# Performance work log

Hardware: AMD Instinct MI355X
Metric: run time of the kernel (lower is better)

Reference implementation:

```python
import jax, jax.numpy as jnp
import numpy as np

B, N, E = 32, 128, 16384
D, H, O, A = 72, 72, 72, 4   # n_input, n_hidden, n_output, n_node_attr
C_WEIGHT = 1.0
EPS = 1e-5  # BatchNorm1d default eps


def setup_inputs() -> dict:
    key = jax.random.key(0)
    ks = jax.random.split(key, 16)
    rn = lambda k, shp, s=0.05: jax.random.normal(k, shp, jnp.float32) * s
    return {
        "h": jax.random.normal(ks[0], (B, N, D), jnp.float32),
        "x": jax.random.normal(ks[1], (B, N, 4), jnp.float32),
        "edgei": jax.random.randint(ks[2], (B, E), 0, N),
        "edgej": jax.random.randint(ks[3], (B, E), 0, N),
        "node_attr": jax.random.normal(ks[4], (B, N, A), jnp.float32),
        # phi_e: Linear(2D+2 -> H, no bias), BN, ReLU, Linear(H->H), ReLU
        "We1": rn(ks[5], (2 * D + 2, H)),
        "g1": jnp.ones((H,), jnp.float32), "b1": jnp.zeros((H,), jnp.float32),
        "We2": rn(ks[6], (H, H)), "be2": jnp.zeros((H,), jnp.float32),
        # phi_m: Linear(H->1), Sigmoid
        "Wm": rn(ks[7], (H, 1)), "bm": jnp.zeros((1,), jnp.float32),
        # phi_x: Linear(H->H), ReLU, Linear(H->1, no bias, tiny init)
        "Wx1": rn(ks[8], (H, H)), "bx1": jnp.zeros((H,), jnp.float32),
        "Wx2": rn(ks[9], (H, 1), 0.001),
        # phi_h: Linear(H+D+A -> H), BN, ReLU, Linear(H->O)
        "Wh1": rn(ks[10], (H + D + A, H)), "bh1": jnp.zeros((H,), jnp.float32),
        "gh": jnp.ones((H,), jnp.float32), "bh": jnp.zeros((H,), jnp.float32),
        "Wh2": rn(ks[11], (H, O)), "bh2": jnp.zeros((O,), jnp.float32),
    }


def _psi(p):
    return jnp.sign(p) * jnp.log1p(jnp.abs(p))


def _normsq4(p):  # Minkowski norm: p0^2 - p1^2 - p2^2 - p3^2
    psq = p * p
    return 2.0 * psq[..., 0] - psq.sum(axis=-1)


def _dotsq4(p, q):  # Minkowski inner product
    pq = p * q
    return 2.0 * pq[..., 0] - pq.sum(axis=-1)


def _batchnorm(z, g, b):  # training-mode BatchNorm1d over flattened batch dim
    mu = z.mean(axis=0)
    var = z.var(axis=0)
    return (z - mu) * jax.lax.rsqrt(var + EPS) * g + b


_seg_sum = jax.vmap(lambda d, s: jax.ops.segment_sum(d, s, num_segments=N))


def reference(h, x, edgei, edgej, node_attr,
              We1, g1, b1, We2, be2, Wm, bm,
              Wx1, bx1, Wx2, Wh1, bh1, gh, bh, Wh2, bh2):
    # gather edge endpoint features (equiv. to torch.gather along dim 1)
    xi = jnp.take_along_axis(x, edgei[:, :, None], axis=1)    # [B,E,4]
    xj = jnp.take_along_axis(x, edgej[:, :, None], axis=1)
    hi = jnp.take_along_axis(h, edgei[:, :, None], axis=1)    # [B,E,D]
    hj = jnp.take_along_axis(h, edgej[:, :, None], axis=1)
    x_diff = xi - xj
    norms = _psi(_normsq4(x_diff))[..., None]                 # [B,E,1]
    dots = _psi(_dotsq4(xi, xj))[..., None]                   # [B,E,1]

    # m_model: phi_e then sigmoid gate phi_m
    feat = jnp.concatenate([hi, hj, norms, dots], axis=-1)    # [B,E,2D+2]
    z = feat.reshape(-1, 2 * D + 2) @ We1
    z = jax.nn.relu(_batchnorm(z, g1, b1))
    z = jax.nn.relu(z @ We2 + be2)
    m = z.reshape(B, E, H)
    m = m * jax.nn.sigmoid(m @ Wm + bm)                       # gated messages

    # x_model: equivariant coordinate update (segment mean over edges)
    gate = jax.nn.relu(m @ Wx1 + bx1) @ Wx2                   # [B,E,1]
    trans = jnp.clip(x_diff * gate, -100.0, 100.0)
    agg = _seg_sum(trans, edgei)                              # [B,N,4]
    cnt = _seg_sum(jnp.ones_like(trans), edgei)
    x_out = x + (agg / jnp.maximum(cnt, 1.0)) * C_WEIGHT

    # h_model: segment sum of messages, node MLP, residual
    magg = _seg_sum(m, edgei)                                 # [B,N,H]
    hin = jnp.concatenate([h, magg, node_attr], axis=-1).reshape(-1, H + D + A)
    z2 = hin @ Wh1 + bh1
    z2 = jax.nn.relu(_batchnorm(z2, gh, bh))
    z2 = z2 @ Wh2 + bh2
    h_out = h + z2.reshape(B, N, O)

    return (h_out, x_out, m)
```

## Files before the change

### kernel.cpp

```cpp
#include <hip/hip_runtime.h>

#define BB 32
#define NN 128
#define EE 16384
#define ROWS_E (BB*EE)
#define ROWS_N (BB*NN)
#define EPS_BN 1e-5f

#define XOUT_OFF (ROWS_N*72)
#define M_OFF    (XOUT_OFF + ROWS_N*4)

#define ST1_OFF 0
#define ST2_OFF 512
#define AGG_OFF 1024
#define CNT_OFF (AGG_OFF + ROWS_N*4)
#define MAGG_OFF (CNT_OFF + ROWS_N)
#define Z2_OFF (MAGG_OFF + ROWS_N*72)
#define ZERO_FLOATS Z2_OFF
#define WB_OFF (Z2_OFF + ROWS_N*72)

#define WE1T_OFF 0
#define WE2T_OFF 13440
#define WX1T_OFF 21760
#define WH1T_OFF 30080
#define WH2T_OFF 43520
#define WB_TOTAL 51840

typedef __attribute__((ext_vector_type(8))) short short8;
typedef __attribute__((ext_vector_type(4))) float f32x4;

__device__ __forceinline__ float psi_f(float p) {
    return copysignf(log1pf(fabsf(p)), p);
}
__device__ __forceinline__ unsigned short f2bf(float f) {
    union { float f; unsigned u; } v; v.f = f;
    unsigned r = v.u + 0x7fffu + ((v.u >> 16) & 1u);
    return (unsigned short)(r >> 16);
}
__device__ __forceinline__ unsigned pk(float a, float b) {
    return (unsigned)f2bf(a) | ((unsigned)f2bf(b) << 16);
}

__global__ void k_prep(const float* __restrict__ We1, const float* __restrict__ We2,
                       const float* __restrict__ Wx1, const float* __restrict__ Wh1,
                       const float* __restrict__ Wh2, unsigned short* __restrict__ wb)
{
    int idx = blockIdx.x * 256 + threadIdx.x;
    if (idx >= WB_TOTAL) return;
    const float* src; int off, n, k, K;
    if (idx < WE2T_OFF)      { off = idx;            n = off/168; k = off%168; src = We1; K = 146; }
    else if (idx < WH1T_OFF && idx >= WX1T_OFF) { off = idx - WX1T_OFF; n = off/104; k = off%104; src = Wx1; K = 72; }
    else if (idx < WX1T_OFF) { off = idx - WE2T_OFF; n = off/104; k = off%104; src = We2; K = 72; }
    else if (idx < WH2T_OFF) { off = idx - WH1T_OFF; n = off/168; k = off%168; src = Wh1; K = 148; }
    else                     { off = idx - WH2T_OFF; n = off/104; k = off%104; src = Wh2; K = 72; }
    float v = (n < 72 && k < K) ? src[k * 72 + n] : 0.f;
    wb[idx] = f2bf(v);
}

__global__ __launch_bounds__(256) void k_edge_gemm1(
    const float* __restrict__ h, const float* __restrict__ x,
    const int* __restrict__ ei, const int* __restrict__ ej,
    const unsigned short* __restrict__ We1t, float* __restrict__ z1)
{
    __shared__ unsigned short At[128 * 168];
    __shared__ unsigned short Wt[80 * 168];
    int tid = threadIdx.x;
    {
        const uint4* s = (const uint4*)We1t; uint4* d = (uint4*)Wt;
        for (int q = tid; q < 1680; q += 256) d[q] = s[q];
    }
    int rl = tid >> 1, half = tid & 1;
    int row = blockIdx.x * 128 + rl;
    int b = row >> 14;
    int i = ei[row], j = ej[row];
    int node = half ? j : i;
    const float4* hp = (const float4*)(h + (size_t)(b * 128 + node) * 72);
    uint2* arow = (uint2*)(&At[rl * 168 + half * 72]);
    #pragma unroll
    for (int q = 0; q < 18; q++) {
        float4 v = hp[q];
        arow[q] = make_uint2(pk(v.x, v.y), pk(v.z, v.w));
    }
    unsigned* tailp = (unsigned*)(&At[rl * 168 + 146]);
    if (half == 0) {
        float4 xi = *(const float4*)(x + (size_t)(b * 128 + i) * 4);
        float4 xj = *(const float4*)(x + (size_t)(b * 128 + j) * 4);
        float d0 = xi.x - xj.x, d1 = xi.y - xj.y, d2 = xi.z - xj.z, d3 = xi.w - xj.w;
        float nrm = d0*d0 - d1*d1 - d2*d2 - d3*d3;
        float dot = xi.x*xj.x - xi.y*xj.y - xi.z*xj.z - xi.w*xj.w;
        *(unsigned*)(&At[rl * 168 + 144]) = pk(psi_f(nrm), psi_f(dot));
        #pragma unroll
        for (int q = 0; q < 6; q++) tailp[q] = 0u;
    } else {
        #pragma unroll
        for (int q = 6; q < 11; q++) tailp[q] = 0u;
    }
    __syncthreads();

    int wv = tid >> 6, lane = tid & 63, c = lane & 15, quad = lane >> 4;
    f32x4 acc[2][5] = {};
    for (int kc = 0; kc < 5; kc++) {
        int k0 = kc * 32 + quad * 8;
        short8 a0 = *(const short8*)(&At[(wv * 32 + c) * 168 + k0]);
        short8 a1 = *(const short8*)(&At[(wv * 32 + 16 + c) * 168 + k0]);
        #pragma unroll
        for (int ct = 0; ct < 5; ct++) {
            short8 bf = *(const short8*)(&Wt[(ct * 16 + c) * 168 + k0]);
            acc[0][ct] = __builtin_amdgcn_mfma_f32_16x16x32_bf16(a0, bf, acc[0][ct], 0, 0, 0);
            acc[1][ct] = __builtin_amdgcn_mfma_f32_16x16x32_bf16(a1, bf, acc[1][ct], 0, 0, 0);
        }
    }
    size_t rbase = (size_t)blockIdx.x * 128 + wv * 32 + quad * 4;
    #pragma unroll
    for (int rt = 0; rt < 2; rt++)
        #pragma unroll
        for (int ct = 0; ct < 5; ct++) {
            int col = ct * 16 + c;
            if (col < 72) {
                float* op = z1 + (rbase + rt * 16) * 72 + col;
                #pragma unroll
                for (int r = 0; r < 4; r++) op[(size_t)r * 72] = acc[rt][ct][r];
            }
        }
}

__global__ void k_stats(const float* __restrict__ z, int rows, float* __restrict__ st)
{
    __shared__ float ssum[4][72];
    __shared__ float ssq[4][72];
    int c = threadIdx.x, ty = threadIdx.y;
    float s = 0.f, q = 0.f;
    for (int r = blockIdx.x * 4 + ty; r < rows; r += gridDim.x * 4) {
        float v = z[(size_t)r * 72 + c];
        s += v; q += v * v;
    }
    ssum[ty][c] = s; ssq[ty][c] = q;
    __syncthreads();
    if (ty == 0) {
        s = ssum[0][c] + ssum[1][c] + ssum[2][c] + ssum[3][c];
        q = ssq[0][c] + ssq[1][c] + ssq[2][c] + ssq[3][c];
        atomicAdd(&st[c], s);
        atomicAdd(&st[72 + c], q);
    }
}

__global__ void k_finalize(float* __restrict__ st, float inv_rows)
{
    int c = threadIdx.x;
    if (c < 72) {
        float mean = st[c] * inv_rows;
        float var  = st[72 + c] * inv_rows - mean * mean;
        st[144 + c] = mean;
        st[216 + c] = rsqrtf(var + EPS_BN);
    }
}

__global__ __launch_bounds__(256) void k_edge_main(
    const float* __restrict__ x, const int* __restrict__ ei, const int* __restrict__ ej,
    const float* __restrict__ st1, const float* __restrict__ g1, const float* __restrict__ b1,
    const float* __restrict__ be2, const float* __restrict__ Wm, const float* __restrict__ bm,
    const float* __restrict__ bx1, const float* __restrict__ Wx2,
    const unsigned short* __restrict__ We2t, const unsigned short* __restrict__ Wx1t,
    float* __restrict__ m, float* __restrict__ agg, float* __restrict__ cnt)
{
    __shared__ unsigned short Zt[128 * 104];
    __shared__ unsigned short W2[80 * 104];
    __shared__ unsigned short W3[80 * 104];
    __shared__ float g2buf[128];
    int tid = threadIdx.x;
    {
        const uint4* s2 = (const uint4*)We2t; uint4* d2 = (uint4*)W2;
        const uint4* s3 = (const uint4*)Wx1t; uint4* d3 = (uint4*)W3;
        for (int q = tid; q < 1040; q += 256) { d2[q] = s2[q]; d3[q] = s3[q]; }
    }
    int rl = tid >> 1, half = tid & 1;
    size_t row = (size_t)blockIdx.x * 128 + rl;
    const float* mean = st1 + 144;
    const float* inv  = st1 + 216;
    const float4* zp = (const float4*)(m + row * 72) + half * 9;
    uint2* arow = (uint2*)(&Zt[rl * 104 + half * 36]);
    #pragma unroll
    for (int q = 0; q < 9; q++) {
        int k = half * 36 + q * 4;
        float4 v = zp[q];
        float a0 = fmaxf((v.x - mean[k  ]) * inv[k  ] * g1[k  ] + b1[k  ], 0.f);
        float a1 = fmaxf((v.y - mean[k+1]) * inv[k+1] * g1[k+1] + b1[k+1], 0.f);
        float a2 = fmaxf((v.z - mean[k+2]) * inv[k+2] * g1[k+2] + b1[k+2], 0.f);
        float a3 = fmaxf((v.w - mean[k+3]) * inv[k+3] * g1[k+3] + b1[k+3], 0.f);
        arow[q] = make_uint2(pk(a0, a1), pk(a2, a3));
    }
    uint2* prow = (uint2*)(&Zt[rl * 104]);
    #pragma unroll
    for (int q = 0; q < 4; q++) prow[18 + half * 4 + q] = make_uint2(0u, 0u);
    __syncthreads();

    int wv = tid >> 6, lane = tid & 63, c = lane & 15, quad = lane >> 4;
    f32x4 acc2[2][5] = {};
    for (int kc = 0; kc < 3; kc++) {
        int k0 = kc * 32 + quad * 8;
        short8 a0 = *(const short8*)(&Zt[(wv * 32 + c) * 104 + k0]);
        short8 a1 = *(const short8*)(&Zt[(wv * 32 + 16 + c) * 104 + k0]);
        #pragma unroll
        for (int ct = 0; ct < 5; ct++) {
            short8 bf = *(const short8*)(&W2[(ct * 16 + c) * 104 + k0]);
            acc2[0][ct] = __builtin_amdgcn_mfma_f32_16x16x32_bf16(a0, bf, acc2[0][ct], 0, 0, 0);
            acc2[1][ct] = __builtin_amdgcn_mfma_f32_16x16x32_bf16(a1, bf, acc2[1][ct], 0, 0, 0);
        }
    }
    float part[2][4] = {};
    float bm0 = bm[0];
    #pragma unroll
    for (int ct = 0; ct < 5; ct++) {
        int col = ct * 16 + c;
        float bias = (col < 72) ? be2[col] : 0.f;
        float wm   = (col < 72) ? Wm[col]  : 0.f;
        #pragma unroll
        for (int rt = 0; rt < 2; rt++)
            #pragma unroll
            for (int r = 0; r < 4; r++) {
                float t = fmaxf(acc2[rt][ct][r] + bias, 0.f);
                acc2[rt][ct][r] = t;
                part[rt][r] += t * wm;
            }
    }
    float sg[2][4];
    #pragma unroll
    for (int rt = 0; rt < 2; rt++)
        #pragma unroll
        for (int r = 0; r < 4; r++) {
            float s = part[rt][r];
            s += __shfl_xor(s, 1); s += __shfl_xor(s, 2);
            s += __shfl_xor(s, 4); s += __shfl_xor(s, 8);
            sg[rt][r] = 1.f / (1.f + expf(-(s + bm0)));
        }
    size_t rbase = (size_t)blockIdx.x * 128 + wv * 32 + quad * 4;
    #pragma unroll
    for (int rt = 0; rt < 2; rt++)
        #pragma unroll
        for (int ct = 0; ct < 5; ct++) {
            int col = ct * 16 + c;
            #pragma unroll
            for (int r = 0; r < 4; r++) {
                float mv = acc2[rt][ct][r] * sg[rt][r];
                int lrow = wv * 32 + rt * 16 + quad * 4 + r;
                Zt[lrow * 104 + col] = f2bf(mv);
                if (col < 72) m[(rbase + rt * 16 + r) * 72 + col] = mv;
            }
        }
    f32x4 acc3[2][5] = {};
    for (int kc = 0; kc < 3; kc++) {
        int k0 = kc * 32 + quad * 8;
        short8 a0 = *(const short8*)(&Zt[(wv * 32 + c) * 104 + k0]);
        short8 a1 = *(const short8*)(&Zt[(wv * 32 + 16 + c) * 104 + k0]);
        #pragma unroll
        for (int ct = 0; ct < 5; ct++) {
            short8 bf = *(const short8*)(&W3[(ct * 16 + c) * 104 + k0]);
            acc3[0][ct] = __builtin_amdgcn_mfma_f32_16x16x32_bf16(a0, bf, acc3[0][ct], 0, 0, 0);
            acc3[1][ct] = __builtin_amdgcn_mfma_f32_16x16x32_bf16(a1, bf, acc3[1][ct], 0, 0, 0);
        }
    }
    float part3[2][4] = {};
    #pragma unroll
    for (int ct = 0; ct < 5; ct++) {
        int col = ct * 16 + c;
        float bias = (col < 72) ? bx1[col] : 0.f;
        float wx   = (col < 72) ? Wx2[col] : 0.f;
        #pragma unroll
        for (int rt = 0; rt < 2; rt++)
            #pragma unroll
            for (int r = 0; r < 4; r++)
                part3[rt][r] += fmaxf(acc3[rt][ct][r] + bias, 0.f) * wx;
    }
    #pragma unroll
    for (int rt = 0; rt < 2; rt++)
        #pragma unroll
        for (int r = 0; r < 4; r++) {
            float s = part3[rt][r];
            s += __shfl_xor(s, 1); s += __shfl_xor(s, 2);
            s += __shfl_xor(s, 4); s += __shfl_xor(s, 8);
            if (c == 0) g2buf[wv * 32 + rt * 16 + quad * 4 + r] = s;
        }
    __syncthreads();
    if (tid < 128) {
        size_t erow = (size_t)blockIdx.x * 128 + tid;
        int b = (int)(erow >> 14);
        int i2 = ei[erow], j2 = ej[erow];
        float g2 = g2buf[tid];
        float4 xi = *(const float4*)(x + (size_t)(b * 128 + i2) * 4);
        float4 xj = *(const float4*)(x + (size_t)(b * 128 + j2) * 4);
        float t0 = fminf(fmaxf((xi.x - xj.x) * g2, -100.f), 100.f);
        float t1 = fminf(fmaxf((xi.y - xj.y) * g2, -100.f), 100.f);
        float t2 = fminf(fmaxf((xi.z - xj.z) * g2, -100.f), 100.f);
        float t3 = fminf(fmaxf((xi.w - xj.w) * g2, -100.f), 100.f);
        float* ap = agg + (size_t)(b * 128 + i2) * 4;
        atomicAdd(ap + 0, t0); atomicAdd(ap + 1, t1);
        atomicAdd(ap + 2, t2); atomicAdd(ap + 3, t3);
        atomicAdd(cnt + (size_t)(b * 128 + i2), 1.f);
    }
}

__global__ __launch_bounds__(256) void k_magg(
    const float* __restrict__ m, const int* __restrict__ ei, float* __restrict__ magg)
{
    __shared__ float accum[128 * 72];
    int tid = threadIdx.x;
    for (int q = tid; q < 9216; q += 256) accum[q] = 0.f;
    __syncthreads();
    int b = blockIdx.x >> 3, chunk = blockIdx.x & 7;
    int wv = tid >> 6, lane = tid & 63;
    int ebase = b * 16384 + chunk * 2048;
    for (int e = wv; e < 2048; e += 4) {
        int erow = ebase + e;
        int node = ei[erow];
        const float* mr = m + (size_t)erow * 72;
        atomicAdd(&accum[node * 72 + lane], mr[lane]);
        if (lane < 8) atomicAdd(&accum[node * 72 + 64 + lane], mr[64 + lane]);
    }
    __syncthreads();
    float* mg = magg + (size_t)b * 9216;
    for (int q = tid; q < 9216; q += 256) atomicAdd(&mg[q], accum[q]);
}

__global__ __launch_bounds__(256) void k_node_gemm1(
    const float* __restrict__ h, const float* __restrict__ node_attr,
    const float* __restrict__ magg, const unsigned short* __restrict__ Wh1t,
    const float* __restrict__ bh1, float* __restrict__ z2)
{
    __shared__ unsigned short At[128 * 168];
    __shared__ unsigned short Wt[80 * 168];
    int tid = threadIdx.x;
    {
        const uint4* s = (const uint4*)Wh1t; uint4* d = (uint4*)Wt;
        for (int q = tid; q < 1680; q += 256) d[q] = s[q];
    }
    int rl = tid >> 1, half = tid & 1;
    size_t row = (size_t)blockIdx.x * 128 + rl;
    const float4* sp = (const float4*)((half ? magg : h) + row * 72);
    uint2* arow = (uint2*)(&At[rl * 168 + half * 72]);
    #pragma unroll
    for (int q = 0; q < 18; q++) {
        float4 v = sp[q];
        arow[q] = make_uint2(pk(v.x, v.y), pk(v.z, v.w));
    }
    if (half) {
        float4 na = *(const float4*)(node_attr + row * 4);
        *(unsigned*)(&At[rl * 168 + 144]) = pk(na.x, na.y);
        *(unsigned*)(&At[rl * 168 + 146]) = pk(na.z, na.w);
        unsigned* tailp = (unsigned*)(&At[rl * 168 + 148]);
        #pragma unroll
        for (int q = 0; q < 10; q++) tailp[q] = 0u;
    }
    __syncthreads();

    int wv = tid >> 6, lane = tid & 63, c = lane & 15, quad = lane >> 4;
    f32x4 acc[2][5] = {};
    for (int kc = 0; kc < 5; kc++) {
        int k0 = kc * 32 + quad * 8;
        short8 a0 = *(const short8*)(&At[(wv * 32 + c) * 168 + k0]);
        short8 a1 = *(const short8*)(&At[(wv * 32 + 16 + c) * 168 + k0]);
        #pragma unroll
        for (int ct = 0; ct < 5; ct++) {
            short8 bf = *(const short8*)(&Wt[(ct * 16 + c) * 168 + k0]);
            acc[0][ct] = __builtin_amdgcn_mfma_f32_16x16x32_bf16(a0, bf, acc[0][ct], 0, 0, 0);
            acc[1][ct] = __builtin_amdgcn_mfma_f32_16x16x32_bf16(a1, bf, acc[1][ct], 0, 0, 0);
        }
    }
    size_t rbase = (size_t)blockIdx.x * 128 + wv * 32 + quad * 4;
    #pragma unroll
    for (int rt = 0; rt < 2; rt++)
        #pragma unroll
        for (int ct = 0; ct < 5; ct++) {
            int col = ct * 16 + c;
            if (col < 72) {
                float bias = bh1[col];
                float* op = z2 + (rbase + rt * 16) * 72 + col;
                #pragma unroll
                for (int r = 0; r < 4; r++) op[(size_t)r * 72] = acc[rt][ct][r] + bias;
            }
        }
}

__global__ __launch_bounds__(256) void k_node_final(
    const float* __restrict__ h, const float* __restrict__ x,
    const float* __restrict__ z2, const float* __restrict__ st2,
    const float* __restrict__ gh, const float* __restrict__ bh,
    const unsigned short* __restrict__ Wh2t, const float* __restrict__ bh2,
    const float* __restrict__ agg, const float* __restrict__ cnt,
    float* __restrict__ hout, float* __restrict__ xout)
{
    __shared__ unsigned short Zt[128 * 104];
    __shared__ unsigned short Wt[80 * 104];
    int tid = threadIdx.x;
    {
        const uint4* s = (const uint4*)Wh2t; uint4* d = (uint4*)Wt;
        for (int q = tid; q < 1040; q += 256) d[q] = s[q];
    }
    int rl = tid >> 1, half = tid & 1;
    size_t row = (size_t)blockIdx.x * 128 + rl;
    const float* mean = st2 + 144;
    const float* inv  = st2 + 216;
    const float4* zp = (const float4*)(z2 + row * 72) + half * 9;
    uint2* arow = (uint2*)(&Zt[rl * 104 + half * 36]);
    #pragma unroll
    for (int q = 0; q < 9; q++) {
        int k = half * 36 + q * 4;
        float4 v = zp[q];
        float a0 = fmaxf((v.x - mean[k  ]) * inv[k  ] * gh[k  ] + bh[k  ], 0.f);
        float a1 = fmaxf((v.y - mean[k+1]) * inv[k+1] * gh[k+1] + bh[k+1], 0.f);
        float a2 = fmaxf((v.z - mean[k+2]) * inv[k+2] * gh[k+2] + bh[k+2], 0.f);
        float a3 = fmaxf((v.w - mean[k+3]) * inv[k+3] * gh[k+3] + bh[k+3], 0.f);
        arow[q] = make_uint2(pk(a0, a1), pk(a2, a3));
    }
    uint2* prow = (uint2*)(&Zt[rl * 104]);
    #pragma unroll
    for (int q = 0; q < 4; q++) prow[18 + half * 4 + q] = make_uint2(0u, 0u);
    __syncthreads();

    int wv = tid >> 6, lane = tid & 63, c = lane & 15, quad = lane >> 4;
    f32x4 acc[2][5] = {};
    for (int kc = 0; kc < 3; kc++) {
        int k0 = kc * 32 + quad * 8;
        short8 a0 = *(const short8*)(&Zt[(wv * 32 + c) * 104 + k0]);
        short8 a1 = *(const short8*)(&Zt[(wv * 32 + 16 + c) * 104 + k0]);
        #pragma unroll
        for (int ct = 0; ct < 5; ct++) {
            short8 bf = *(const short8*)(&Wt[(ct * 16 + c) * 104 + k0]);
            acc[0][ct] = __builtin_amdgcn_mfma_f32_16x16x32_bf16(a0, bf, acc[0][ct], 0, 0, 0);
            acc[1][ct] = __builtin_amdgcn_mfma_f32_16x16x32_bf16(a1, bf, acc[1][ct], 0, 0, 0);
        }
    }
    size_t rbase = (size_t)blockIdx.x * 128 + wv * 32 + quad * 4;
    #pragma unroll
    for (int rt = 0; rt < 2; rt++)
        #pragma unroll
        for (int ct = 0; ct < 5; ct++) {
            int col = ct * 16 + c;
            if (col < 72) {
                float bias = bh2[col];
                #pragma unroll
                for (int r = 0; r < 4; r++) {
                    size_t gr = (rbase + rt * 16 + r);
                    hout[gr * 72 + col] = h[gr * 72 + col] + acc[rt][ct][r] + bias;
                }
            }
        }
    if (tid < 128) {
        size_t nrow = (size_t)blockIdx.x * 128 + tid;
        float cn = fmaxf(cnt[nrow], 1.f);
        float4 ag = *(const float4*)(agg + nrow * 4);
        float4 xv = *(const float4*)(x + nrow * 4);
        ((float4*)xout)[nrow] = make_float4(xv.x + ag.x / cn, xv.y + ag.y / cn,
                                            xv.z + ag.z / cn, xv.w + ag.w / cn);
    }
}

extern "C" void kernel_launch(void* const* d_in, const int* in_sizes, int n_in,
                              void* d_out, int out_size, void* d_ws, size_t ws_size,
                              hipStream_t stream)
{
    const float* h   = (const float*)d_in[0];
    const float* x   = (const float*)d_in[1];
    const int*   ei  = (const int*)d_in[2];
    const int*   ej  = (const int*)d_in[3];
    const float* na  = (const float*)d_in[4];
    const float* We1 = (const float*)d_in[5];
    const float* g1  = (const float*)d_in[6];
    const float* b1  = (const float*)d_in[7];
    const float* We2 = (const float*)d_in[8];
    const float* be2 = (const float*)d_in[9];
    const float* Wm  = (const float*)d_in[10];
    const float* bm  = (const float*)d_in[11];
    const float* Wx1 = (const float*)d_in[12];
    const float* bx1 = (const float*)d_in[13];
    const float* Wx2 = (const float*)d_in[14];
    const float* Wh1 = (const float*)d_in[15];
    const float* bh1 = (const float*)d_in[16];
    const float* gh  = (const float*)d_in[17];
    const float* bhp = (const float*)d_in[18];
    const float* Wh2 = (const float*)d_in[19];
    const float* bh2 = (const float*)d_in[20];

    float* out  = (float*)d_out;
    float* hout = out;
    float* xout = out + XOUT_OFF;
    float* m    = out + M_OFF;
    float* ws   = (float*)d_ws;
    float* st1  = ws + ST1_OFF;
    float* st2  = ws + ST2_OFF;
    float* agg  = ws + AGG_OFF;
    float* cnt  = ws + CNT_OFF;
    float* magg = ws + MAGG_OFF;
    float* z2   = ws + Z2_OFF;
    unsigned short* wb = (unsigned short*)(ws + WB_OFF);

    hipMemsetAsync(d_ws, 0, (size_t)ZERO_FLOATS * sizeof(float), stream);
    k_prep<<<(WB_TOTAL + 255) / 256, 256, 0, stream>>>(We1, We2, Wx1, Wh1, Wh2, wb);
    k_edge_gemm1<<<ROWS_E / 128, 256, 0, stream>>>(h, x, ei, ej, wb + WE1T_OFF, m);
    k_stats<<<dim3(1024), dim3(72, 4), 0, stream>>>(m, ROWS_E, st1);
    k_finalize<<<1, 128, 0, stream>>>(st1, 1.0f / (float)ROWS_E);
    k_edge_main<<<ROWS_E / 128, 256, 0, stream>>>(x, ei, ej, st1, g1, b1, be2, Wm, bm,
                                                  bx1, Wx2, wb + WE2T_OFF, wb + WX1T_OFF,
                                                  m, agg, cnt);
    k_magg<<<256, 256, 0, stream>>>(m, ei, magg);
    k_node_gemm1<<<ROWS_N / 128, 256, 0, stream>>>(h, na, magg, wb + WH1T_OFF, bh1, z2);
    k_stats<<<dim3(16), dim3(72, 4), 0, stream>>>(z2, ROWS_N, st2);
    k_finalize<<<1, 128, 0, stream>>>(st2, 1.0f / (float)ROWS_N);
    k_node_final<<<ROWS_N / 128, 256, 0, stream>>>(h, x, z2, st2, gh, bhp,
                                                   wb + WH2T_OFF, bh2, agg, cnt, hout, xout);
}
```

Before: 783.0 us.

## Store BN pre-activations in bf16 and feed MFMA operands from registers

The edge GEMM kernels now gather edge features straight into MFMA B-operand registers in transposed (weight-as-A) form, and read weights from global memory. This removes the big LDS staging tiles and their syncs. When the workspace is large enough, the first-layer pre-activation z1 goes to a separate bf16 buffer instead of fp32 in the output. That halves the traffic for the stats pass and for the edge_main read, with a new bf16 stats kernel. BatchNorm scale and shift are folded into per-channel S/T in finalize. The trade-off is that stats are computed on rounded bf16 values, and weights are fetched from global or cache instead of LDS.

```diff
diff --git a/kernel.cpp b/kernel.cpp
--- a/kernel.cpp
+++ b/kernel.cpp
@@ -1,4 +1,5 @@
 #include <hip/hip_runtime.h>
+#include <hip/hip_bf16.h>
 
 #define BB 32
 #define NN 128
@@ -18,6 +19,8 @@
 #define Z2_OFF (MAGG_OFF + ROWS_N*72)
 #define ZERO_FLOATS Z2_OFF
 #define WB_OFF (Z2_OFF + ROWS_N*72)
+#define Z1BF_OFF 637248
+#define Z1BF_NEED ((size_t)(Z1BF_OFF + ROWS_E*72/2) * 4)
 
 #define WE1T_OFF 0
 #define WE2T_OFF 13440
@@ -38,7 +41,12 @@
     return (unsigned short)(r >> 16);
 }
 __device__ __forceinline__ unsigned pk(float a, float b) {
-    return (unsigned)f2bf(a) | ((unsigned)f2bf(b) << 16);
+    union { __hip_bfloat162 h; unsigned u; } cv;
+    cv.h = __float22bfloat162_rn(make_float2(a, b));
+    return cv.u;
+}
+__device__ __forceinline__ float bfu2f(unsigned u) {
+    union { unsigned u; float f; } v; v.u = u << 16; return v.f;
 }
 
 __global__ void k_prep(const float* __restrict__ We1, const float* __restrict__ We2,
@@ -47,81 +55,100 @@
 {
     int idx = blockIdx.x * 256 + threadIdx.x;
     if (idx >= WB_TOTAL) return;
-    const float* src; int off, n, k, K;
-    if (idx < WE2T_OFF)      { off = idx;            n = off/168; k = off%168; src = We1; K = 146; }
-    else if (idx < WH1T_OFF && idx >= WX1T_OFF) { off = idx - WX1T_OFF; n = off/104; k = off%104; src = Wx1; K = 72; }
-    else if (idx < WX1T_OFF) { off = idx - WE2T_OFF; n = off/104; k = off%104; src = We2; K = 72; }
-    else if (idx < WH2T_OFF) { off = idx - WH1T_OFF; n = off/168; k = off%168; src = Wh1; K = 148; }
-    else                     { off = idx - WH2T_OFF; n = off/104; k = off%104; src = Wh2; K = 72; }
+    const float* src; int off = idx, n, k, K;
+    if (off < WE2T_OFF)      {                  n = off/168; k = off%168; src = We1; K = 146; }
+    else if (off < WX1T_OFF) { off -= WE2T_OFF; n = off/104; k = off%104; src = We2; K = 72; }
+    else if (off < WH1T_OFF) { off -= WX1T_OFF; n = off/104; k = off%104; src = Wx1; K = 72; }
+    else if (off < WH2T_OFF) { off -= WH1T_OFF; n = off/168; k = off%168; src = Wh1; K = 148; }
+    else                     { off -= WH2T_OFF; n = off/104; k = off%104; src = Wh2; K = 72; }
     float v = (n < 72 && k < K) ? src[k * 72 + n] : 0.f;
     wb[idx] = f2bf(v);
 }
 
+template<bool BF>
 __global__ __launch_bounds__(256) void k_edge_gemm1(
     const float* __restrict__ h, const float* __restrict__ x,
     const int* __restrict__ ei, const int* __restrict__ ej,
-    const unsigned short* __restrict__ We1t, float* __restrict__ z1)
-{
-    __shared__ unsigned short At[128 * 168];
-    __shared__ unsigned short Wt[80 * 168];
+    const unsigned short* __restrict__ We1t, void* __restrict__ z1v)
+{
     int tid = threadIdx.x;
-    {
-        const uint4* s = (const uint4*)We1t; uint4* d = (uint4*)Wt;
-        for (int q = tid; q < 1680; q += 256) d[q] = s[q];
-    }
-    int rl = tid >> 1, half = tid & 1;
-    int row = blockIdx.x * 128 + rl;
-    int b = row >> 14;
-    int i = ei[row], j = ej[row];
-    int node = half ? j : i;
-    const float4* hp = (const float4*)(h + (size_t)(b * 128 + node) * 72);
-    uint2* arow = (uint2*)(&At[rl * 168 + half * 72]);
-    #pragma unroll
-    for (int q = 0; q < 18; q++) {
-        float4 v = hp[q];
-        arow[q] = make_uint2(pk(v.x, v.y), pk(v.z, v.w));
-    }
-    unsigned* tailp = (unsigned*)(&At[rl * 168 + 146]);
-    if (half == 0) {
-        float4 xi = *(const float4*)(x + (size_t)(b * 128 + i) * 4);
-        float4 xj = *(const float4*)(x + (size_t)(b * 128 + j) * 4);
-        float d0 = xi.x - xj.x, d1 = xi.y - xj.y, d2 = xi.z - xj.z, d3 = xi.w - xj.w;
-        float nrm = d0*d0 - d1*d1 - d2*d2 - d3*d3;
-        float dot = xi.x*xj.x - xi.y*xj.y - xi.z*xj.z - xi.w*xj.w;
-        *(unsigned*)(&At[rl * 168 + 144]) = pk(psi_f(nrm), psi_f(dot));
-        #pragma unroll
-        for (int q = 0; q < 6; q++) tailp[q] = 0u;
-    } else {
-        #pragma unroll
-        for (int q = 6; q < 11; q++) tailp[q] = 0u;
-    }
-    __syncthreads();
-
     int wv = tid >> 6, lane = tid & 63, c = lane & 15, quad = lane >> 4;
+    int blk = blockIdx.x;
+    int b = blk >> 7;
+    size_t ebase = (size_t)blk * 128 + wv * 32;
+    const float* hb = h + (size_t)b * 128 * 72;
+
+    int iN[2], jN[2];
+    #pragma unroll
+    for (int nt = 0; nt < 2; nt++) {
+        size_t e = ebase + nt * 16 + c;
+        iN[nt] = ei[e]; jN[nt] = ej[e];
+    }
+
     f32x4 acc[2][5] = {};
+    #pragma unroll
     for (int kc = 0; kc < 5; kc++) {
         int k0 = kc * 32 + quad * 8;
-        short8 a0 = *(const short8*)(&At[(wv * 32 + c) * 168 + k0]);
-        short8 a1 = *(const short8*)(&At[(wv * 32 + 16 + c) * 168 + k0]);
-        #pragma unroll
-        for (int ct = 0; ct < 5; ct++) {
-            short8 bf = *(const short8*)(&Wt[(ct * 16 + c) * 168 + k0]);
-            acc[0][ct] = __builtin_amdgcn_mfma_f32_16x16x32_bf16(a0, bf, acc[0][ct], 0, 0, 0);
-            acc[1][ct] = __builtin_amdgcn_mfma_f32_16x16x32_bf16(a1, bf, acc[1][ct], 0, 0, 0);
-        }
-    }
-    size_t rbase = (size_t)blockIdx.x * 128 + wv * 32 + quad * 4;
-    #pragma unroll
-    for (int rt = 0; rt < 2; rt++)
-        #pragma unroll
-        for (int ct = 0; ct < 5; ct++) {
-            int col = ct * 16 + c;
-            if (col < 72) {
-                float* op = z1 + (rbase + rt * 16) * 72 + col;
-                #pragma unroll
-                for (int r = 0; r < 4; r++) op[(size_t)r * 72] = acc[rt][ct][r];
+        int ch = kc * 4 + quad;
+        short8 bfr[2];
+        #pragma unroll
+        for (int nt = 0; nt < 2; nt++) {
+            if (ch < 18) {
+                const float* p = hb + (ch < 9 ? iN[nt] * 72 + ch * 8
+                                              : jN[nt] * 72 + (ch - 9) * 8);
+                float4 p0 = *(const float4*)p;
+                float4 p1 = *(const float4*)(p + 4);
+                short8 t;
+                unsigned u0 = pk(p0.x, p0.y), u1 = pk(p0.z, p0.w);
+                unsigned u2 = pk(p1.x, p1.y), u3 = pk(p1.z, p1.w);
+                t[0] = (short)(u0 & 0xffff); t[1] = (short)(u0 >> 16);
+                t[2] = (short)(u1 & 0xffff); t[3] = (short)(u1 >> 16);
+                t[4] = (short)(u2 & 0xffff); t[5] = (short)(u2 >> 16);
+                t[6] = (short)(u3 & 0xffff); t[7] = (short)(u3 >> 16);
+                bfr[nt] = t;
+            } else if (ch == 18) {
+                float4 xi = *(const float4*)(x + (size_t)(b * 128 + iN[nt]) * 4);
+                float4 xj = *(const float4*)(x + (size_t)(b * 128 + jN[nt]) * 4);
+                float d0 = xi.x-xj.x, d1 = xi.y-xj.y, d2 = xi.z-xj.z, d3 = xi.w-xj.w;
+                float nrm = d0*d0 - d1*d1 - d2*d2 - d3*d3;
+                float dot = xi.x*xj.x - xi.y*xj.y - xi.z*xj.z - xi.w*xj.w;
+                unsigned u = pk(psi_f(nrm), psi_f(dot));
+                short8 t = {0,0,0,0,0,0,0,0};
+                t[0] = (short)(u & 0xffff); t[1] = (short)(u >> 16);
+                bfr[nt] = t;
+            } else {
+                short8 t = {0,0,0,0,0,0,0,0};
+                bfr[nt] = t;
             }
         }
+        #pragma unroll
+        for (int mt = 0; mt < 5; mt++) {
+            short8 w = *(const short8*)(We1t + (mt * 16 + c) * 168 + k0);
+            acc[0][mt] = __builtin_amdgcn_mfma_f32_16x16x32_bf16(w, bfr[0], acc[0][mt], 0, 0, 0);
+            acc[1][mt] = __builtin_amdgcn_mfma_f32_16x16x32_bf16(w, bfr[1], acc[1][mt], 0, 0, 0);
+        }
+    }
+    #pragma unroll
+    for (int nt = 0; nt < 2; nt++) {
+        size_t e = ebase + nt * 16 + c;
+        #pragma unroll
+        for (int mt = 0; mt < 5; mt++) {
+            int col0 = mt * 16 + quad * 4;
+            if (col0 < 72) {
+                if (BF) {
+                    unsigned short* z1bf = (unsigned short*)z1v;
+                    *(uint2*)(z1bf + e * 72 + col0) =
+                        make_uint2(pk(acc[nt][mt][0], acc[nt][mt][1]),
+                                   pk(acc[nt][mt][2], acc[nt][mt][3]));
+                } else {
+                    float* z1f = (float*)z1v;
+                    *(float4*)(z1f + e * 72 + col0) =
+                        make_float4(acc[nt][mt][0], acc[nt][mt][1],
+                                    acc[nt][mt][2], acc[nt][mt][3]);
+                }
+            }
+        }
+    }
 }
 
 __global__ void k_stats(const float* __restrict__ z, int rows, float* __restrict__ st)
@@ -144,148 +171,210 @@
     }
 }
 
-__global__ void k_finalize(float* __restrict__ st, float inv_rows)
+__global__ void k_stats_bf(const unsigned* __restrict__ z1u, float* __restrict__ st)
+{
+    __shared__ float ssum[7][72];
+    __shared__ float ssq[7][72];
+    int p = threadIdx.x;
+    int ty = threadIdx.y;
+    float s0 = 0.f, s1 = 0.f, q0 = 0.f, q1 = 0.f;
+    for (int r = blockIdx.x * 7 + ty; r < ROWS_E; r += gridDim.x * 7) {
+        unsigned v = z1u[(size_t)r * 36 + p];
+        float a = bfu2f(v & 0xffffu);
+        float bb = bfu2f(v >> 16);
+        s0 += a; q0 += a * a; s1 += bb; q1 += bb * bb;
+    }
+    ssum[ty][2*p] = s0; ssum[ty][2*p+1] = s1;
+    ssq[ty][2*p] = q0;  ssq[ty][2*p+1] = q1;
+    __syncthreads();
+    if (ty == 0) {
+        #pragma unroll
+        for (int hh = 0; hh < 2; hh++) {
+            int col = 2*p + hh;
+            float s = 0.f, q = 0.f;
+            #pragma unroll
+            for (int t = 0; t < 7; t++) { s += ssum[t][col]; q += ssq[t][col]; }
+            atomicAdd(&st[col], s);
+            atomicAdd(&st[72 + col], q);
+        }
+    }
+}
+
+__global__ void k_finalize(float* __restrict__ st, float inv_rows,
+                           const float* __restrict__ g, const float* __restrict__ b)
 {
     int c = threadIdx.x;
     if (c < 72) {
         float mean = st[c] * inv_rows;
         float var  = st[72 + c] * inv_rows - mean * mean;
+        float rst  = rsqrtf(var + EPS_BN);
         st[144 + c] = mean;
-        st[216 + c] = rsqrtf(var + EPS_BN);
-    }
-}
-
+        st[216 + c] = rst;
+        float S = rst * g[c];
+        st[288 + c] = S;
+        st[360 + c] = b[c] - mean * S;
+    }
+}
+
+template<bool BF>
 __global__ __launch_bounds__(256) void k_edge_main(
-    const float* __restrict__ x, const int* __restrict__ ei, const int* __restrict__ ej,
-    const float* __restrict__ st1, const float* __restrict__ g1, const float* __restrict__ b1,
-    const float* __restrict__ be2, const float* __restrict__ Wm, const float* __restrict__ bm,
+    const void* __restrict__ z1v, const float* __restrict__ x,
+    const int* __restrict__ ei, const int* __restrict__ ej,
+    const float* __restrict__ st1, const float* __restrict__ be2,
+    const float* __restrict__ Wm, const float* __restrict__ bm,
     const float* __restrict__ bx1, const float* __restrict__ Wx2,
     const unsigned short* __restrict__ We2t, const unsigned short* __restrict__ Wx1t,
     float* __restrict__ m, float* __restrict__ agg, float* __restrict__ cnt)
 {
-    __shared__ unsigned short Zt[128 * 104];
-    __shared__ unsigned short W2[80 * 104];
-    __shared__ unsigned short W3[80 * 104];
-    __shared__ float g2buf[128];
+    __shared__ unsigned short mtile[128 * 72];
     int tid = threadIdx.x;
-    {
-        const uint4* s2 = (const uint4*)We2t; uint4* d2 = (uint4*)W2;
-        const uint4* s3 = (const uint4*)Wx1t; uint4* d3 = (uint4*)W3;
-        for (int q = tid; q < 1040; q += 256) { d2[q] = s2[q]; d3[q] = s3[q]; }
-    }
-    int rl = tid >> 1, half = tid & 1;
-    size_t row = (size_t)blockIdx.x * 128 + rl;
-    const float* mean = st1 + 144;
-    const float* inv  = st1 + 216;
-    const float4* zp = (const float4*)(m + row * 72) + half * 9;
-    uint2* arow = (uint2*)(&Zt[rl * 104 + half * 36]);
-    #pragma unroll
-    for (int q = 0; q < 9; q++) {
-        int k = half * 36 + q * 4;
-        float4 v = zp[q];
-        float a0 = fmaxf((v.x - mean[k  ]) * inv[k  ] * g1[k  ] + b1[k  ], 0.f);
-        float a1 = fmaxf((v.y - mean[k+1]) * inv[k+1] * g1[k+1] + b1[k+1], 0.f);
-        float a2 = fmaxf((v.z - mean[k+2]) * inv[k+2] * g1[k+2] + b1[k+2], 0.f);
-        float a3 = fmaxf((v.w - mean[k+3]) * inv[k+3] * g1[k+3] + b1[k+3], 0.f);
-        arow[q] = make_uint2(pk(a0, a1), pk(a2, a3));
-    }
-    uint2* prow = (uint2*)(&Zt[rl * 104]);
-    #pragma unroll
-    for (int q = 0; q < 4; q++) prow[18 + half * 4 + q] = make_uint2(0u, 0u);
-    __syncthreads();
-
     int wv = tid >> 6, lane = tid & 63, c = lane & 15, quad = lane >> 4;
-    f32x4 acc2[2][5] = {};
+    int blk = blockIdx.x;
+    int b = blk >> 7;
+    size_t ebase = (size_t)blk * 128 + wv * 32;
+    const float* Sp = st1 + 288;
+    const float* Tp = st1 + 360;
+
+    short8 zb[2][3];
+    #pragma unroll
     for (int kc = 0; kc < 3; kc++) {
         int k0 = kc * 32 + quad * 8;
-        short8 a0 = *(const short8*)(&Zt[(wv * 32 + c) * 104 + k0]);
-        short8 a1 = *(const short8*)(&Zt[(wv * 32 + 16 + c) * 104 + k0]);
-        #pragma unroll
-        for (int ct = 0; ct < 5; ct++) {
-            short8 bf = *(const short8*)(&W2[(ct * 16 + c) * 104 + k0]);
-            acc2[0][ct] = __builtin_amdgcn_mfma_f32_16x16x32_bf16(a0, bf, acc2[0][ct], 0, 0, 0);
-            acc2[1][ct] = __builtin_amdgcn_mfma_f32_16x16x32_bf16(a1, bf, acc2[1][ct], 0, 0, 0);
-        }
-    }
-    float part[2][4] = {};
-    float bm0 = bm[0];
-    #pragma unroll
-    for (int ct = 0; ct < 5; ct++) {
-        int col = ct * 16 + c;
-        float bias = (col < 72) ? be2[col] : 0.f;
-        float wm   = (col < 72) ? Wm[col]  : 0.f;
-        #pragma unroll
-        for (int rt = 0; rt < 2; rt++)
+        if (k0 < 72) {
+            float4 Sa = *(const float4*)(Sp + k0), Sb4 = *(const float4*)(Sp + k0 + 4);
+            float4 Ta = *(const float4*)(Tp + k0), Tb4 = *(const float4*)(Tp + k0 + 4);
             #pragma unroll
-            for (int r = 0; r < 4; r++) {
-                float t = fmaxf(acc2[rt][ct][r] + bias, 0.f);
-                acc2[rt][ct][r] = t;
-                part[rt][r] += t * wm;
+            for (int nt = 0; nt < 2; nt++) {
+                size_t e = ebase + nt * 16 + c;
+                float v0,v1,v2,v3,v4,v5,v6,v7;
+                if (BF) {
+                    const unsigned* z1u = (const unsigned*)z1v;
+                    uint4 u = *(const uint4*)(z1u + e * 36 + (k0 >> 1));
+                    v0 = bfu2f(u.x & 0xffffu); v1 = bfu2f(u.x >> 16);
+                    v2 = bfu2f(u.y & 0xffffu); v3 = bfu2f(u.y >> 16);
+                    v4 = bfu2f(u.z & 0xffffu); v5 = bfu2f(u.z >> 16);
+                    v6 = bfu2f(u.w & 0xffffu); v7 = bfu2f(u.w >> 16);
+                } else {
+                    const float* z1f = (const float*)z1v;
+                    float4 p0 = *(const float4*)(z1f + e * 72 + k0);
+                    float4 p1 = *(const float4*)(z1f + e * 72 + k0 + 4);
+                    v0 = p0.x; v1 = p0.y; v2 = p0.z; v3 = p0.w;
+                    v4 = p1.x; v5 = p1.y; v6 = p1.z; v7 = p1.w;
+                }
+                float a0 = fmaxf(v0*Sa.x + Ta.x, 0.f), a1 = fmaxf(v1*Sa.y + Ta.y, 0.f);
+                float a2 = fmaxf(v2*Sa.z + Ta.z, 0.f), a3 = fmaxf(v3*Sa.w + Ta.w, 0.f);
+                float a4 = fmaxf(v4*Sb4.x + Tb4.x, 0.f), a5 = fmaxf(v5*Sb4.y + Tb4.y, 0.f);
+                float a6 = fmaxf(v6*Sb4.z + Tb4.z, 0.f), a7 = fmaxf(v7*Sb4.w + Tb4.w, 0.f);
+                unsigned u0 = pk(a0,a1), u1 = pk(a2,a3), u2 = pk(a4,a5), u3 = pk(a6,a7);
+                short8 t;
+                t[0]=(short)(u0&0xffff); t[1]=(short)(u0>>16);
+                t[2]=(short)(u1&0xffff); t[3]=(short)(u1>>16);
+                t[4]=(short)(u2&0xffff); t[5]=(short)(u2>>16);
+                t[6]=(short)(u3&0xffff); t[7]=(short)(u3>>16);
+                zb[nt][kc] = t;
             }
-    }
-    float sg[2][4];
-    #pragma unroll
-    for (int rt = 0; rt < 2; rt++)
-        #pragma unroll
-        for (int r = 0; r < 4; r++) {
-            float s = part[rt][r];
-            s += __shfl_xor(s, 1); s += __shfl_xor(s, 2);
-            s += __shfl_xor(s, 4); s += __shfl_xor(s, 8);
-            sg[rt][r] = 1.f / (1.f + expf(-(s + bm0)));
-        }
-    size_t rbase = (size_t)blockIdx.x * 128 + wv * 32 + quad * 4;
-    #pragma unroll
-    for (int rt = 0; rt < 2; rt++)
-        #pragma unroll
-        for (int ct = 0; ct < 5; ct++) {
-            int col = ct * 16 + c;
-            #pragma unroll
-            for (int r = 0; r < 4; r++) {
-                float mv = acc2[rt][ct][r] * sg[rt][r];
-                int lrow = wv * 32 + rt * 16 + quad * 4 + r;
-                Zt[lrow * 104 + col] = f2bf(mv);
-                if (col < 72) m[(rbase + rt * 16 + r) * 72 + col] = mv;
-            }
-        }
-    f32x4 acc3[2][5] = {};
+        } else {
+            short8 t = {0,0,0,0,0,0,0,0};
+            zb[0][kc] = t; zb[1][kc] = t;
+        }
+    }
+
+    f32x4 acc2[2][5] = {};
+    #pragma unroll
     for (int kc = 0; kc < 3; kc++) {
         int k0 = kc * 32 + quad * 8;
-        short8 a0 = *(const short8*)(&Zt[(wv * 32 + c) * 104 + k0]);
-        short8 a1 = *(const short8*)(&Zt[(wv * 32 + 16 + c) * 104 + k0]);
-        #pragma unroll
-        for (int ct = 0; ct < 5; ct++) {
-            short8 bf = *(const short8*)(&W3[(ct * 16 + c) * 104 + k0]);
-            acc3[0][ct] = __builtin_amdgcn_mfma_f32_16x16x32_bf16(a0, bf, acc3[0][ct], 0, 0, 0);
-            acc3[1][ct] = __builtin_amdgcn_mfma_f32_16x16x32_bf16(a1, bf, acc3[1][ct], 0, 0, 0);
-        }
-    }
-    float part3[2][4] = {};
-    #pragma unroll
-    for (int ct = 0; ct < 5; ct++) {
-        int col = ct * 16 + c;
-        float bias = (col < 72) ? bx1[col] : 0.f;
-        float wx   = (col < 72) ? Wx2[col] : 0.f;
-        #pragma unroll
-        for (int rt = 0; rt < 2; rt++)
-            #pragma unroll
-            for (int r = 0; r < 4; r++)
-                part3[rt][r] += fmaxf(acc3[rt][ct][r] + bias, 0.f) * wx;
-    }
-    #pragma unroll
-    for (int rt = 0; rt < 2; rt++)
-        #pragma unroll
-        for (int r = 0; r < 4; r++) {
-            float s = part3[rt][r];
-            s += __shfl_xor(s, 1); s += __shfl_xor(s, 2);
-            s += __shfl_xor(s, 4); s += __shfl_xor(s, 8);
-            if (c == 0) g2buf[wv * 32 + rt * 16 + quad * 4 + r] = s;
-        }
-    __syncthreads();
-    if (tid < 128) {
-        size_t erow = (size_t)blockIdx.x * 128 + tid;
-        int b = (int)(erow >> 14);
-        int i2 = ei[erow], j2 = ej[erow];
-        float g2 = g2buf[tid];
+        #pragma unroll
+        for (int mt = 0; mt < 5; mt++) {
+            short8 w = *(const short8*)(We2t + (mt * 16 + c) * 104 + k0);
+            acc2[0][mt] = __builtin_amdgcn_mfma_f32_16x16x32_bf16(w, zb[0][kc], acc2[0][mt], 0, 0, 0);
+            acc2[1][mt] = __builtin_amdgcn_mfma_f32_16x16x32_bf16(w, zb[1][kc], acc2[1][mt], 0, 0, 0);
+        }
+    }
+    float part[2] = {0.f, 0.f};
+    #pragma unroll
+    for (int mt = 0; mt < 5; mt++) {
+        int col0 = mt * 16 + quad * 4;
+        float4 be = make_float4(0,0,0,0), wm = make_float4(0,0,0,0);
+        if (col0 < 72) { be = *(const float4*)(be2 + col0); wm = *(const float4*)(Wm + col0); }
+        #pragma unroll
+        for (int nt = 0; nt < 2; nt++) {
+            float t0 = fmaxf(acc2[nt][mt][0] + be.x, 0.f);
+            float t1 = fmaxf(acc2[nt][mt][1] + be.y, 0.f);
+            float t2 = fmaxf(acc2[nt][mt][2] + be.z, 0.f);
+            float t3 = fmaxf(acc2[nt][mt][3] + be.w, 0.f);
+            acc2[nt][mt][0] = t0; acc2[nt][mt][1] = t1;
+            acc2[nt][mt][2] = t2; acc2[nt][mt][3] = t3;
+            part[nt] += t0*wm.x + t1*wm.y + t2*wm.z + t3*wm.w;
+        }
+    }
+    float bm0 = bm[0];
+    float gate[2];
+    #pragma unroll
+    for (int nt = 0; nt < 2; nt++) {
+        float s = part[nt];
+        s += __shfl_xor(s, 16);
+        s += __shfl_xor(s, 32);
+        gate[nt] = 1.f / (1.f + expf(-(s + bm0)));
+    }
+    #pragma unroll
+    for (int nt = 0; nt < 2; nt++) {
+        size_t e = ebase + nt * 16 + c;
+        int el = wv * 32 + nt * 16 + c;
+        #pragma unroll
+        for (int mt = 0; mt < 5; mt++) {
+            int col0 = mt * 16 + quad * 4;
+            if (col0 < 72) {
+                float m0 = acc2[nt][mt][0] * gate[nt];
+                float m1 = acc2[nt][mt][1] * gate[nt];
+                float m2 = acc2[nt][mt][2] * gate[nt];
+                float m3 = acc2[nt][mt][3] * gate[nt];
+                *(float4*)(m + e * 72 + col0) = make_float4(m0, m1, m2, m3);
+                *(uint2*)(&mtile[el * 72 + col0]) = make_uint2(pk(m0, m1), pk(m2, m3));
+            }
+        }
+    }
+    f32x4 acc3[2][5] = {};
+    #pragma unroll
+    for (int kc = 0; kc < 3; kc++) {
+        int k0 = kc * 32 + quad * 8;
+        short8 mb[2];
+        #pragma unroll
+        for (int nt = 0; nt < 2; nt++) {
+            if (k0 < 72) mb[nt] = *(const short8*)(&mtile[(wv*32 + nt*16 + c) * 72 + k0]);
+            else { short8 t = {0,0,0,0,0,0,0,0}; mb[nt] = t; }
+        }
+        #pragma unroll
+        for (int mt = 0; mt < 5; mt++) {
+            short8 w = *(const short8*)(Wx1t + (mt * 16 + c) * 104 + k0);
+            acc3[0][mt] = __builtin_amdgcn_mfma_f32_16x16x32_bf16(w, mb[0], acc3[0][mt], 0, 0, 0);
+            acc3[1][mt] = __builtin_amdgcn_mfma_f32_16x16x32_bf16(w, mb[1], acc3[1][mt], 0, 0, 0);
+        }
+    }
+    float part3[2] = {0.f, 0.f};
+    #pragma unroll
+    for (int mt = 0; mt < 5; mt++) {
+        int col0 = mt * 16 + quad * 4;
+        float4 bx = make_float4(0,0,0,0), wx = make_float4(0,0,0,0);
+        if (col0 < 72) { bx = *(const float4*)(bx1 + col0); wx = *(const float4*)(Wx2 + col0); }
+        #pragma unroll
+        for (int nt = 0; nt < 2; nt++) {
+            part3[nt] += fmaxf(acc3[nt][mt][0] + bx.x, 0.f) * wx.x
+                       + fmaxf(acc3[nt][mt][1] + bx.y, 0.f) * wx.y
+                       + fmaxf(acc3[nt][mt][2] + bx.z, 0.f) * wx.z
+                       + fmaxf(acc3[nt][mt][3] + bx.w, 0.f) * wx.w;
+        }
+    }
+    float g2v[2];
+    #pragma unroll
+    for (int nt = 0; nt < 2; nt++) {
+        float s = part3[nt];
+        s += __shfl_xor(s, 16);
+        s += __shfl_xor(s, 32);
+        g2v[nt] = s;
+    }
+    if (quad < 2) {
+        size_t e = ebase + quad * 16 + c;
+        float g2 = quad ? g2v[1] : g2v[0];
+        int i2 = ei[e], j2 = ej[e];
         float4 xi = *(const float4*)(x + (size_t)(b * 128 + i2) * 4);
         float4 xj = *(const float4*)(x + (size_t)(b * 128 + j2) * 4);
         float t0 = fminf(fmaxf((xi.x - xj.x) * g2, -100.f), 100.f);
@@ -360,9 +449,9 @@
         short8 a1 = *(const short8*)(&At[(wv * 32 + 16 + c) * 168 + k0]);
         #pragma unroll
         for (int ct = 0; ct < 5; ct++) {
-            short8 bf = *(const short8*)(&Wt[(ct * 16 + c) * 168 + k0]);
-            acc[0][ct] = __builtin_amdgcn_mfma_f32_16x16x32_bf16(a0, bf, acc[0][ct], 0, 0, 0);
-            acc[1][ct] = __builtin_amdgcn_mfma_f32_16x16x32_bf16(a1, bf, acc[1][ct], 0, 0, 0);
+            short8 bfw = *(const short8*)(&Wt[(ct * 16 + c) * 168 + k0]);
+            acc[0][ct] = __builtin_amdgcn_mfma_f32_16x16x32_bf16(a0, bfw, acc[0][ct], 0, 0, 0);
+            acc[1][ct] = __builtin_amdgcn_mfma_f32_16x16x32_bf16(a1, bfw, acc[1][ct], 0, 0, 0);
         }
     }
     size_t rbase = (size_t)blockIdx.x * 128 + wv * 32 + quad * 4;
@@ -424,9 +513,9 @@
         short8 a1 = *(const short8*)(&Zt[(wv * 32 + 16 + c) * 104 + k0]);
         #pragma unroll
         for (int ct = 0; ct < 5; ct++) {
-            short8 bf = *(const short8*)(&Wt[(ct * 16 + c) * 104 + k0]);
-            acc[0][ct] = __builtin_amdgcn_mfma_f32_16x16x32_bf16(a0, bf, acc[0][ct], 0, 0, 0);
-            acc[1][ct] = __builtin_amdgcn_mfma_f32_16x16x32_bf16(a1, bf, acc[1][ct], 0, 0, 0);
+            short8 bfw = *(const short8*)(&Wt[(ct * 16 + c) * 104 + k0]);
+            acc[0][ct] = __builtin_amdgcn_mfma_f32_16x16x32_bf16(a0, bfw, acc[0][ct], 0, 0, 0);
+            acc[1][ct] = __builtin_amdgcn_mfma_f32_16x16x32_bf16(a1, bfw, acc[1][ct], 0, 0, 0);
         }
     }
     size_t rbase = (size_t)blockIdx.x * 128 + wv * 32 + quad * 4;
@@ -492,19 +581,34 @@
     float* magg = ws + MAGG_OFF;
     float* z2   = ws + Z2_OFF;
     unsigned short* wb = (unsigned short*)(ws + WB_OFF);
+    unsigned short* z1bf = (unsigned short*)(ws + Z1BF_OFF);
+
+    bool bf = ws_size >= Z1BF_NEED;
+    void* z1v = bf ? (void*)z1bf : (void*)m;
 
     hipMemsetAsync(d_ws, 0, (size_t)ZERO_FLOATS * sizeof(float), stream);
     k_prep<<<(WB_TOTAL + 255) / 256, 256, 0, stream>>>(We1, We2, Wx1, Wh1, Wh2, wb);
-    k_edge_gemm1<<<ROWS_E / 128, 256, 0, stream>>>(h, x, ei, ej, wb + WE1T_OFF, m);
-    k_stats<<<dim3(1024), dim3(72, 4), 0, stream>>>(m, ROWS_E, st1);
-    k_finalize<<<1, 128, 0, stream>>>(st1, 1.0f / (float)ROWS_E);
-    k_edge_main<<<ROWS_E / 128, 256, 0, stream>>>(x, ei, ej, st1, g1, b1, be2, Wm, bm,
-                                                  bx1, Wx2, wb + WE2T_OFF, wb + WX1T_OFF,
-                                                  m, agg, cnt);
+    if (bf) {
+        k_edge_gemm1<true><<<ROWS_E / 128, 256, 0, stream>>>(h, x, ei, ej, wb + WE1T_OFF, z1v);
+        k_stats_bf<<<2048, dim3(36, 7), 0, stream>>>((const unsigned*)z1bf, st1);
+    } else {
+        k_edge_gemm1<false><<<ROWS_E / 128, 256, 0, stream>>>(h, x, ei, ej, wb + WE1T_OFF, z1v);
+        k_stats<<<2048, dim3(72, 4), 0, stream>>>((const float*)z1v, ROWS_E, st1);
+    }
+    k_finalize<<<1, 128, 0, stream>>>(st1, 1.0f / (float)ROWS_E, g1, b1);
+    if (bf) {
+        k_edge_main<true><<<ROWS_E / 128, 256, 0, stream>>>(z1v, x, ei, ej, st1, be2, Wm, bm,
+                                                            bx1, Wx2, wb + WE2T_OFF, wb + WX1T_OFF,
+                                                            m, agg, cnt);
+    } else {
+        k_edge_main<false><<<ROWS_E / 128, 256, 0, stream>>>(z1v, x, ei, ej, st1, be2, Wm, bm,
+                                                             bx1, Wx2, wb + WE2T_OFF, wb + WX1T_OFF,
+                                                             m, agg, cnt);
+    }
     k_magg<<<256, 256, 0, stream>>>(m, ei, magg);
     k_node_gemm1<<<ROWS_N / 128, 256, 0, stream>>>(h, na, magg, wb + WH1T_OFF, bh1, z2);
-    k_stats<<<dim3(16), dim3(72, 4), 0, stream>>>(z2, ROWS_N, st2);
-    k_finalize<<<1, 128, 0, stream>>>(st2, 1.0f / (float)ROWS_N);
+    k_stats<<<16, dim3(72, 4), 0, stream>>>(z2, ROWS_N, st2);
+    k_finalize<<<1, 128, 0, stream>>>(st2, 1.0f / (float)ROWS_N, gh, bhp);
     k_node_final<<<ROWS_N / 128, 256, 0, stream>>>(h, x, z2, st2, gh, bhp,
                                                    wb + WH2T_OFF, bh2, agg, cnt, hout, xout);
 }
```

Measured after the change: 820.5 us. 4.8% more time.
